# Kernel tuning notes

Measured on AMD Instinct MI355X. Metric: run time of the kernel, lower is better.

The kernel has to match this reference:

```python
import jax, jax.numpy as jnp
import numpy as np

B, S, D, H, DK, DV = 4, 2048, 512, 8, 64, 64


def setup_inputs() -> dict:
    key0 = jax.random.key(0)
    ks = jax.random.split(key0, 11)
    w = 0.02
    return {
        "query": jax.random.normal(ks[0], (B, S, D), dtype=jnp.float32),
        "key": jax.random.normal(ks[1], (B, S, D), dtype=jnp.float32),
        "value": jax.random.normal(ks[2], (B, S, D), dtype=jnp.float32),
        "Wq": jax.random.normal(ks[3], (D, DK), dtype=jnp.float32) * w,
        "bq": jnp.zeros((DK,), dtype=jnp.float32),
        "Wk": jax.random.normal(ks[4], (D, DK), dtype=jnp.float32) * w,
        "bk": jnp.zeros((DK,), dtype=jnp.float32),
        "Wv": jax.random.normal(ks[5], (D, DV), dtype=jnp.float32) * w,
        "bv": jnp.zeros((DV,), dtype=jnp.float32),
        "Wo": jax.random.normal(ks[6], (H * DV, D), dtype=jnp.float32) * w,
        "bo": jnp.zeros((D,), dtype=jnp.float32),
    }


def reference(query, key, value, Wq, bq, Wk, bk, Wv, bv, Wo, bo):
    # NOTE: original module applies the SAME Dense layers to every head
    # (q_list = [self.query(query) for _ in range(heads)]), so all H heads
    # are mathematically identical -> compute one head and replicate.
    # NOTE: V is projected from `key`, not `value` (faithful to source bug).
    q = query @ Wq + bq          # [B, S, DK]
    k = key @ Wk + bk            # [B, S, DK]
    v = key @ Wv + bv            # [B, S, DV]
    scale = np.sqrt(DK).astype(np.float32)
    scores = jnp.einsum("bqd,bkd->bqk", q, k) / scale  # [B, S, S]
    # masked_mha=True and training=True -> causal mask, fill -1e19
    causal = jnp.triu(jnp.ones((S, S), dtype=scores.dtype), 1)
    scores = scores + causal * jnp.asarray(-1e19, scores.dtype)
    attn = jax.nn.softmax(scores, axis=-1)              # [B, S, S]
    o = jnp.einsum("bqk,bkv->bqv", attn, v)             # [B, S, DV]
    # concat of H identical heads along last axis == tile
    concat = jnp.tile(o, (1, 1, H))                     # [B, S, H*DV]
    return concat @ Wo + bo                             # [B, S, D]
```

## Files before the change

### kernel.cpp

```cpp
#include <hip/hip_runtime.h>
#include <hip/hip_bf16.h>


#define BB 4
#define SS 2048
#define BS (BB*SS)

typedef __bf16          v8bf __attribute__((ext_vector_type(8)));
typedef unsigned short  v8u  __attribute__((ext_vector_type(8)));
typedef float           v4f  __attribute__((ext_vector_type(4)));

__device__ inline unsigned short f2bf(float x) {
    unsigned int u = __float_as_uint(x);
    return (unsigned short)((u + 0x7FFF + ((u >> 16) & 1)) >> 16);
}
__device__ inline float bf2f(unsigned short h) {
    return __uint_as_float((unsigned int)h << 16);
}
union bfcast { v8u u; v8bf b; };

__global__ __launch_bounds__(512) void prep_kernel(
    const float* __restrict__ Wq, const float* __restrict__ bq,
    const float* __restrict__ Wk, const float* __restrict__ bk,
    const float* __restrict__ Wv, const float* __restrict__ bv,
    const float* __restrict__ Wo,
    unsigned short* __restrict__ Wt, float* __restrict__ bs,
    unsigned short* __restrict__ WoEt)
{
    const int t = threadIdx.x, y = blockIdx.y;
    const int idx = blockIdx.x * 512 + t;
    if (y < 3) {
        const float* W  = (y == 0) ? Wq : (y == 1) ? Wk : Wv;
        const float* bb = (y == 0) ? bq : (y == 1) ? bk : bv;
        const float s = (y == 0) ? (0.125f * 1.44269504088896340736f) : 1.0f;
        int c = idx & 63, k = idx >> 6;
        Wt[y * 32768 + c * 512 + k] = f2bf(W[k * 64 + c] * s);
        if (blockIdx.x == 0 && t < 64) bs[y * 64 + t] = bb[t] * s;
    } else {
        int d = idx & 511, k = idx >> 9;
        float sum = 0.f;
#pragma unroll
        for (int h = 0; h < 8; h++) sum += Wo[(size_t)(h * 64 + k) * 512 + d];
        WoEt[d * 64 + k] = f2bf(sum);
    }
}

__global__ __launch_bounds__(256) void proj_kernel(
    const float* __restrict__ query, const float* __restrict__ key,
    const unsigned short* __restrict__ Wt, const float* __restrict__ bs,
    unsigned short* __restrict__ Qp, unsigned short* __restrict__ Kp,
    unsigned short* __restrict__ Vt)
{
    const int t = threadIdx.x;
    const int gw = (blockIdx.x * 256 + t) >> 6;
    const int lane = t & 63, lq = lane & 15, quad = lane >> 4;
    const int src = gw >> 11;
    const int rr  = gw & 2047;
    const int rows = (rr >> 2) * 16;
    const int cb   = (rr & 3) * 16;
    const float* A = (src == 0) ? query : key;
    const unsigned short* W = Wt + src * 32768 + (cb + lq) * 512;
    const float bb = bs[src * 64 + cb + lq];
    v4f acc = {bb, bb, bb, bb};
    const float* arow = A + (size_t)(rows + lq) * 512;

#pragma unroll 4
    for (int k0 = 0; k0 < 512; k0 += 32) {
        float4 f0 = *(const float4*)(arow + k0 + quad * 8);
        float4 f1 = *(const float4*)(arow + k0 + quad * 8 + 4);
        bfcast a;
        a.u[0] = f2bf(f0.x); a.u[1] = f2bf(f0.y); a.u[2] = f2bf(f0.z); a.u[3] = f2bf(f0.w);
        a.u[4] = f2bf(f1.x); a.u[5] = f2bf(f1.y); a.u[6] = f2bf(f1.z); a.u[7] = f2bf(f1.w);
        v8bf b = *(const v8bf*)(W + k0 + quad * 8);
        acc = __builtin_amdgcn_mfma_f32_16x16x32_bf16(a.b, b, acc, 0, 0, 0);
    }

    if (src == 2) {
        ushort4 o4;
        o4.x = f2bf(acc[0]); o4.y = f2bf(acc[1]); o4.z = f2bf(acc[2]); o4.w = f2bf(acc[3]);
        *(ushort4*)&Vt[(size_t)(cb + lq) * BS + rows + quad * 4] = o4;
    } else {
        unsigned short* Out = (src == 0) ? Qp : Kp;
#pragma unroll
        for (int r = 0; r < 4; r++)
            Out[(size_t)(rows + quad * 4 + r) * 64 + cb + lq] = f2bf(acc[r]);
    }
}

__global__ __launch_bounds__(256) void attn_kernel(
    const unsigned short* __restrict__ Qp,
    const unsigned short* __restrict__ Kp,
    const unsigned short* __restrict__ Vt,
    unsigned short* __restrict__ Opart,
    float* __restrict__ mpart, float* __restrict__ lpart,
    int nch)
{
    __shared__ unsigned short Ks[32][72];
    __shared__ unsigned short Vs[64][40];
    __shared__ unsigned short Ps[4][16][40];

    const int t    = threadIdx.x;
    const int lane = t & 63;
    const int w    = t >> 6;
    const int b    = blockIdx.x & 3;
    const int qt   = 31 - (blockIdx.x >> 2);
    const int c    = blockIdx.y;
    const int qbase = qt * 64;
    const int L    = qbase + 64;
    const int cs   = ((L + nch * 32 - 1) / (nch * 32)) * 32;
    const int klo  = c * cs;
    const int khi  = min(klo + cs, L);
    const size_t bbase = (size_t)b * SS;

    const int lq   = lane & 15;
    const int quad = lane >> 4;
    const int qrow_w = qbase + w * 16;
    const int wmax   = qrow_w + 15;

    const size_t qoff = (bbase + qrow_w + lq) * 64;
    v8bf qa0 = *(const v8bf*)(Qp + qoff + quad * 8);
    v8bf qa1 = *(const v8bf*)(Qp + qoff + 32 + quad * 8);

    v4f  o[4] = {};
    float mr[4], lr[4];
#pragma unroll
    for (int r = 0; r < 4; r++) { mr[r] = -1e30f; lr[r] = 0.f; }

    for (int kb = klo; kb < khi; kb += 32) {
        __syncthreads();
        {
            int ky = t >> 3, dd = (t & 7) * 8;
            *(v8bf*)&Ks[ky][dd] = *(const v8bf*)(Kp + (bbase + kb + ky) * 64 + dd);
            int vd = t >> 2, kk = (t & 3) * 8;
            *(v8bf*)&Vs[vd][kk] = *(const v8bf*)(Vt + (size_t)vd * BS + bbase + kb + kk);
        }
        __syncthreads();
        if (kb > wmax) continue;

        v4f s0 = {0.f, 0.f, 0.f, 0.f}, s1 = {0.f, 0.f, 0.f, 0.f};
        {
            v8bf k0a = *(const v8bf*)&Ks[lq][quad * 8];
            v8bf k0b = *(const v8bf*)&Ks[lq][32 + quad * 8];
            v8bf k1a = *(const v8bf*)&Ks[16 + lq][quad * 8];
            v8bf k1b = *(const v8bf*)&Ks[16 + lq][32 + quad * 8];
            s0 = __builtin_amdgcn_mfma_f32_16x16x32_bf16(qa0, k0a, s0, 0, 0, 0);
            s0 = __builtin_amdgcn_mfma_f32_16x16x32_bf16(qa1, k0b, s0, 0, 0, 0);
            s1 = __builtin_amdgcn_mfma_f32_16x16x32_bf16(qa0, k1a, s1, 0, 0, 0);
            s1 = __builtin_amdgcn_mfma_f32_16x16x32_bf16(qa1, k1b, s1, 0, 0, 0);
        }

        const int row0 = qrow_w + quad * 4;
        const int col0 = kb + lq;
        float sc[8];
#pragma unroll
        for (int r = 0; r < 4; r++) {
            sc[r]     = (col0      > row0 + r) ? -1e30f : s0[r];
            sc[4 + r] = (col0 + 16 > row0 + r) ? -1e30f : s1[r];
        }
        float mt[4];
#pragma unroll
        for (int r = 0; r < 4; r++) mt[r] = fmaxf(sc[r], sc[4 + r]);
#pragma unroll
        for (int off = 1; off <= 8; off <<= 1)
#pragma unroll
            for (int r = 0; r < 4; r++) mt[r] = fmaxf(mt[r], __shfl_xor(mt[r], off));

        float al[4], pn[8], ls[4];
#pragma unroll
        for (int r = 0; r < 4; r++) {
            float mn = fmaxf(mr[r], mt[r]);
            al[r] = exp2f(mr[r] - mn);
            mr[r] = mn;
            pn[r]     = exp2f(sc[r]     - mn);
            pn[4 + r] = exp2f(sc[4 + r] - mn);
            ls[r] = pn[r] + pn[4 + r];
        }
#pragma unroll
        for (int off = 1; off <= 8; off <<= 1)
#pragma unroll
            for (int r = 0; r < 4; r++) ls[r] += __shfl_xor(ls[r], off);
#pragma unroll
        for (int r = 0; r < 4; r++) lr[r] = lr[r] * al[r] + ls[r];

#pragma unroll
        for (int r = 0; r < 4; r++) {
            Ps[w][quad * 4 + r][lq]      = f2bf(pn[r]);
            Ps[w][quad * 4 + r][16 + lq] = f2bf(pn[4 + r]);
        }
        v8bf pa = *(const v8bf*)&Ps[w][lq][quad * 8];

#pragma unroll
        for (int vt = 0; vt < 4; vt++) {
            v8bf vb = *(const v8bf*)&Vs[vt * 16 + lq][quad * 8];
#pragma unroll
            for (int r = 0; r < 4; r++) o[vt][r] *= al[r];
            o[vt] = __builtin_amdgcn_mfma_f32_16x16x32_bf16(pa, vb, o[vt], 0, 0, 0);
        }
    }

#pragma unroll
    for (int vt = 0; vt < 4; vt++)
#pragma unroll
        for (int r = 0; r < 4; r++) {
            int qrow = qrow_w + quad * 4 + r;
            Opart[((size_t)c * BS + bbase + qrow) * 64 + vt * 16 + lq] = f2bf(o[vt][r]);
        }
    if (lq < 4) {
        int qrow = qrow_w + quad * 4 + lq;
        float mv = (lq == 0) ? mr[0] : (lq == 1) ? mr[1] : (lq == 2) ? mr[2] : mr[3];
        float lv = (lq == 0) ? lr[0] : (lq == 1) ? lr[1] : (lq == 2) ? lr[2] : lr[3];
        mpart[(size_t)c * BS + bbase + qrow] = mv;
        lpart[(size_t)c * BS + bbase + qrow] = lv;
    }
}

__global__ __launch_bounds__(256) void merge_kernel(
    const unsigned short* __restrict__ Opart, const float* __restrict__ mpart,
    const float* __restrict__ lpart, unsigned short* __restrict__ Om, int nch)
{
    const int idx = blockIdx.x * 256 + threadIdx.x;
    const int row = idx >> 3, dd = (idx & 7) * 8;
    float mm = -1e30f;
    for (int c = 0; c < nch; c++) mm = fmaxf(mm, mpart[(size_t)c * BS + row]);
    float den = 0.f;
    for (int c = 0; c < nch; c++)
        den += exp2f(mpart[(size_t)c * BS + row] - mm) * lpart[(size_t)c * BS + row];
    const float inv = 1.f / den;
    float acc[8] = {};
    for (int c = 0; c < nch; c++) {
        float s = exp2f(mpart[(size_t)c * BS + row] - mm) * inv;
        v8u o = *(const v8u*)&Opart[((size_t)c * BS + row) * 64 + dd];
#pragma unroll
        for (int j = 0; j < 8; j++) acc[j] += s * bf2f(o[j]);
    }
    v8u ou;
#pragma unroll
    for (int j = 0; j < 8; j++) ou[j] = f2bf(acc[j]);
    *(v8u*)&Om[(size_t)row * 64 + dd] = ou;
}

__global__ __launch_bounds__(256) void outgemm_kernel(
    const unsigned short* __restrict__ Om, const unsigned short* __restrict__ WoEt,
    const float* __restrict__ bo, float* __restrict__ out)
{
    const int t = threadIdx.x;
    const int gw = (blockIdx.x * 256 + t) >> 6;
    const int lane = t & 63, lq = lane & 15, quad = lane >> 4;
    const int rows = (gw >> 5) * 16;
    const int cb   = (gw & 31) * 16;

    v8bf a0 = *(const v8bf*)(Om + (size_t)(rows + lq) * 64 + quad * 8);
    v8bf a1 = *(const v8bf*)(Om + (size_t)(rows + lq) * 64 + 32 + quad * 8);
    v8bf b0 = *(const v8bf*)(WoEt + (size_t)(cb + lq) * 64 + quad * 8);
    v8bf b1 = *(const v8bf*)(WoEt + (size_t)(cb + lq) * 64 + 32 + quad * 8);
    const float bb = bo[cb + lq];
    v4f acc = {bb, bb, bb, bb};
    acc = __builtin_amdgcn_mfma_f32_16x16x32_bf16(a0, b0, acc, 0, 0, 0);
    acc = __builtin_amdgcn_mfma_f32_16x16x32_bf16(a1, b1, acc, 0, 0, 0);
#pragma unroll
    for (int r = 0; r < 4; r++)
        out[(size_t)(rows + quad * 4 + r) * 512 + cb + lq] = acc[r];
}

extern "C" void kernel_launch(void* const* d_in, const int* in_sizes, int n_in,
                              void* d_out, int out_size, void* d_ws, size_t ws_size,
                              hipStream_t stream) {
    const float* query = (const float*)d_in[0];
    const float* key   = (const float*)d_in[1];
    const float* Wq = (const float*)d_in[3];
    const float* bq = (const float*)d_in[4];
    const float* Wk = (const float*)d_in[5];
    const float* bk = (const float*)d_in[6];
    const float* Wv = (const float*)d_in[7];
    const float* bv = (const float*)d_in[8];
    const float* Wo = (const float*)d_in[9];
    const float* bo = (const float*)d_in[10];
    float* out = (float*)d_out;

    const int nch = (ws_size >= (size_t)13 * 1024 * 1024) ? 8 : 4;

    char* p = (char*)d_ws;
    unsigned short* Qp    = (unsigned short*)p; p += (size_t)BS * 64 * 2;
    unsigned short* Kp    = (unsigned short*)p; p += (size_t)BS * 64 * 2;
    unsigned short* Vtg   = (unsigned short*)p; p += (size_t)BS * 64 * 2;
    unsigned short* Opart = (unsigned short*)p; p += (size_t)nch * BS * 64 * 2;
    float* mpart = (float*)p; p += (size_t)nch * BS * 4;
    float* lpart = (float*)p; p += (size_t)nch * BS * 4;
    unsigned short* WoEt = (unsigned short*)p; p += (size_t)64 * 512 * 2;
    unsigned short* Wt   = (unsigned short*)p; p += (size_t)3 * 64 * 512 * 2;
    float* bs            = (float*)p;           p += (size_t)3 * 64 * 4;
    unsigned short* Om = Qp;

    prep_kernel<<<dim3(64, 4), 512, 0, stream>>>(Wq, bq, Wk, bk, Wv, bv, Wo, Wt, bs, WoEt);
    proj_kernel<<<1536, 256, 0, stream>>>(query, key, Wt, bs, Qp, Kp, Vtg);
    attn_kernel<<<dim3(128, nch), 256, 0, stream>>>(Qp, Kp, Vtg, Opart, mpart, lpart, nch);
    merge_kernel<<<256, 256, 0, stream>>>(Opart, mpart, lpart, Om, nch);
    outgemm_kernel<<<4096, 256, 0, stream>>>(Om, WoEt, bo, out);
}
```

Measured before the change: 182.1 us.

## Fuse K/V projections, widen attention key tile, merge combine with output GEMM

The projection kernel now computes K and V from the same key rows in one wave, so each key row is loaded and converted to bf16 once instead of twice. The attention kernel processes 64-key tiles instead of 32, which halves the number of barrier-synchronised tile iterations at the cost of larger shared buffers. The split-K merge and the output GEMM are fused into one kernel, which drops a launch and the intermediate Om round trip through global memory. Hand-rolled bf16 rounding is replaced by native __bf16 conversions.

```diff
diff --git a/kernel.cpp b/kernel.cpp
--- a/kernel.cpp
+++ b/kernel.cpp
@@ -6,26 +6,24 @@
 #define SS 2048
 #define BS (BB*SS)
 
-typedef __bf16          v8bf __attribute__((ext_vector_type(8)));
-typedef unsigned short  v8u  __attribute__((ext_vector_type(8)));
-typedef float           v4f  __attribute__((ext_vector_type(4)));
-
-__device__ inline unsigned short f2bf(float x) {
-    unsigned int u = __float_as_uint(x);
-    return (unsigned short)((u + 0x7FFF + ((u >> 16) & 1)) >> 16);
-}
-__device__ inline float bf2f(unsigned short h) {
-    return __uint_as_float((unsigned int)h << 16);
-}
-union bfcast { v8u u; v8bf b; };
+typedef __bf16 v8bf __attribute__((ext_vector_type(8)));
+typedef __bf16 v4bf __attribute__((ext_vector_type(4)));
+typedef float  v4f  __attribute__((ext_vector_type(4)));
+
+__device__ inline v8bf cvt8(float4 f0, float4 f1) {
+    v8bf r;
+    r[0] = (__bf16)f0.x; r[1] = (__bf16)f0.y; r[2] = (__bf16)f0.z; r[3] = (__bf16)f0.w;
+    r[4] = (__bf16)f1.x; r[5] = (__bf16)f1.y; r[6] = (__bf16)f1.z; r[7] = (__bf16)f1.w;
+    return r;
+}
 
 __global__ __launch_bounds__(512) void prep_kernel(
     const float* __restrict__ Wq, const float* __restrict__ bq,
     const float* __restrict__ Wk, const float* __restrict__ bk,
     const float* __restrict__ Wv, const float* __restrict__ bv,
     const float* __restrict__ Wo,
-    unsigned short* __restrict__ Wt, float* __restrict__ bs,
-    unsigned short* __restrict__ WoEt)
+    __bf16* __restrict__ Wt, float* __restrict__ bs,
+    __bf16* __restrict__ WoEt)
 {
     const int t = threadIdx.x, y = blockIdx.y;
     const int idx = blockIdx.x * 512 + t;
@@ -34,70 +32,81 @@
         const float* bb = (y == 0) ? bq : (y == 1) ? bk : bv;
         const float s = (y == 0) ? (0.125f * 1.44269504088896340736f) : 1.0f;
         int c = idx & 63, k = idx >> 6;
-        Wt[y * 32768 + c * 512 + k] = f2bf(W[k * 64 + c] * s);
+        Wt[y * 32768 + c * 512 + k] = (__bf16)(W[k * 64 + c] * s);
         if (blockIdx.x == 0 && t < 64) bs[y * 64 + t] = bb[t] * s;
     } else {
         int d = idx & 511, k = idx >> 9;
         float sum = 0.f;
 #pragma unroll
         for (int h = 0; h < 8; h++) sum += Wo[(size_t)(h * 64 + k) * 512 + d];
-        WoEt[d * 64 + k] = f2bf(sum);
+        WoEt[d * 64 + k] = (__bf16)sum;
     }
 }
 
 __global__ __launch_bounds__(256) void proj_kernel(
     const float* __restrict__ query, const float* __restrict__ key,
-    const unsigned short* __restrict__ Wt, const float* __restrict__ bs,
-    unsigned short* __restrict__ Qp, unsigned short* __restrict__ Kp,
-    unsigned short* __restrict__ Vt)
+    const __bf16* __restrict__ Wt, const float* __restrict__ bs,
+    __bf16* __restrict__ Qp, __bf16* __restrict__ Kp, __bf16* __restrict__ Vt)
 {
     const int t = threadIdx.x;
     const int gw = (blockIdx.x * 256 + t) >> 6;
     const int lane = t & 63, lq = lane & 15, quad = lane >> 4;
-    const int src = gw >> 11;
+    const int kind = gw >> 11;
     const int rr  = gw & 2047;
     const int rows = (rr >> 2) * 16;
     const int cb   = (rr & 3) * 16;
-    const float* A = (src == 0) ? query : key;
-    const unsigned short* W = Wt + src * 32768 + (cb + lq) * 512;
-    const float bb = bs[src * 64 + cb + lq];
-    v4f acc = {bb, bb, bb, bb};
-    const float* arow = A + (size_t)(rows + lq) * 512;
-
+    const float* arow = ((kind == 0) ? query : key) + (size_t)(rows + lq) * 512;
+
+    if (kind == 0) {
+        const __bf16* W = Wt + (cb + lq) * 512;
+        const float bb = bs[cb + lq];
+        v4f acc = {bb, bb, bb, bb};
 #pragma unroll 4
-    for (int k0 = 0; k0 < 512; k0 += 32) {
-        float4 f0 = *(const float4*)(arow + k0 + quad * 8);
-        float4 f1 = *(const float4*)(arow + k0 + quad * 8 + 4);
-        bfcast a;
-        a.u[0] = f2bf(f0.x); a.u[1] = f2bf(f0.y); a.u[2] = f2bf(f0.z); a.u[3] = f2bf(f0.w);
-        a.u[4] = f2bf(f1.x); a.u[5] = f2bf(f1.y); a.u[6] = f2bf(f1.z); a.u[7] = f2bf(f1.w);
-        v8bf b = *(const v8bf*)(W + k0 + quad * 8);
-        acc = __builtin_amdgcn_mfma_f32_16x16x32_bf16(a.b, b, acc, 0, 0, 0);
-    }
-
-    if (src == 2) {
-        ushort4 o4;
-        o4.x = f2bf(acc[0]); o4.y = f2bf(acc[1]); o4.z = f2bf(acc[2]); o4.w = f2bf(acc[3]);
-        *(ushort4*)&Vt[(size_t)(cb + lq) * BS + rows + quad * 4] = o4;
+        for (int k0 = 0; k0 < 512; k0 += 32) {
+            float4 f0 = *(const float4*)(arow + k0 + quad * 8);
+            float4 f1 = *(const float4*)(arow + k0 + quad * 8 + 4);
+            v8bf a = cvt8(f0, f1);
+            v8bf b = *(const v8bf*)(W + k0 + quad * 8);
+            acc = __builtin_amdgcn_mfma_f32_16x16x32_bf16(a, b, acc, 0, 0, 0);
+        }
+#pragma unroll
+        for (int r = 0; r < 4; r++)
+            Qp[(size_t)(rows + quad * 4 + r) * 64 + cb + lq] = (__bf16)acc[r];
     } else {
-        unsigned short* Out = (src == 0) ? Qp : Kp;
+        const __bf16* Wk_ = Wt + 32768  + (cb + lq) * 512;
+        const __bf16* Wv_ = Wt + 65536  + (cb + lq) * 512;
+        const float bk_ = bs[64 + cb + lq], bv_ = bs[128 + cb + lq];
+        v4f ak = {bk_, bk_, bk_, bk_}, av = {bv_, bv_, bv_, bv_};
+#pragma unroll 4
+        for (int k0 = 0; k0 < 512; k0 += 32) {
+            float4 f0 = *(const float4*)(arow + k0 + quad * 8);
+            float4 f1 = *(const float4*)(arow + k0 + quad * 8 + 4);
+            v8bf a  = cvt8(f0, f1);
+            v8bf b0 = *(const v8bf*)(Wk_ + k0 + quad * 8);
+            v8bf b1 = *(const v8bf*)(Wv_ + k0 + quad * 8);
+            ak = __builtin_amdgcn_mfma_f32_16x16x32_bf16(a, b0, ak, 0, 0, 0);
+            av = __builtin_amdgcn_mfma_f32_16x16x32_bf16(a, b1, av, 0, 0, 0);
+        }
 #pragma unroll
         for (int r = 0; r < 4; r++)
-            Out[(size_t)(rows + quad * 4 + r) * 64 + cb + lq] = f2bf(acc[r]);
+            Kp[(size_t)(rows + quad * 4 + r) * 64 + cb + lq] = (__bf16)ak[r];
+        v4bf o4; o4[0] = (__bf16)av[0]; o4[1] = (__bf16)av[1];
+        o4[2] = (__bf16)av[2]; o4[3] = (__bf16)av[3];
+        *(v4bf*)&Vt[(size_t)(cb + lq) * BS + rows + quad * 4] = o4;
     }
 }
 
 __global__ __launch_bounds__(256) void attn_kernel(
-    const unsigned short* __restrict__ Qp,
-    const unsigned short* __restrict__ Kp,
-    const unsigned short* __restrict__ Vt,
-    unsigned short* __restrict__ Opart,
+    const __bf16* __restrict__ Qp,
+    const __bf16* __restrict__ Kp,
+    const __bf16* __restrict__ Vt,
+    __bf16* __restrict__ Opart,
     float* __restrict__ mpart, float* __restrict__ lpart,
     int nch)
 {
-    __shared__ unsigned short Ks[32][72];
-    __shared__ unsigned short Vs[64][40];
-    __shared__ unsigned short Ps[4][16][40];
+    __shared__ __bf16 Ks[64][72];
+    __shared__ __bf16 Vs[64][72];
+    __shared__ __bf16 Ps[4][16][72];
 
     const int t    = threadIdx.x;
     const int lane = t & 63;
@@ -107,7 +116,7 @@
     const int c    = blockIdx.y;
     const int qbase = qt * 64;
     const int L    = qbase + 64;
-    const int cs   = ((L + nch * 32 - 1) / (nch * 32)) * 32;
+    const int cs   = ((L + nch * 64 - 1) / (nch * 64)) * 64;
     const int klo  = c * cs;
     const int khi  = min(klo + cs, L);
     const size_t bbase = (size_t)b * SS;
@@ -126,54 +135,56 @@
 #pragma unroll
     for (int r = 0; r < 4; r++) { mr[r] = -1e30f; lr[r] = 0.f; }
 
-    for (int kb = klo; kb < khi; kb += 32) {
+    for (int kb = klo; kb < khi; kb += 64) {
         __syncthreads();
-        {
-            int ky = t >> 3, dd = (t & 7) * 8;
+#pragma unroll
+        for (int i = 0; i < 2; i++) {
+            int idx = t + i * 256;
+            int ky = idx >> 3, dd = (idx & 7) * 8;
             *(v8bf*)&Ks[ky][dd] = *(const v8bf*)(Kp + (bbase + kb + ky) * 64 + dd);
-            int vd = t >> 2, kk = (t & 3) * 8;
-            *(v8bf*)&Vs[vd][kk] = *(const v8bf*)(Vt + (size_t)vd * BS + bbase + kb + kk);
+            *(v8bf*)&Vs[ky][dd] = *(const v8bf*)(Vt + (size_t)ky * BS + bbase + kb + dd);
         }
         __syncthreads();
         if (kb > wmax) continue;
 
-        v4f s0 = {0.f, 0.f, 0.f, 0.f}, s1 = {0.f, 0.f, 0.f, 0.f};
-        {
-            v8bf k0a = *(const v8bf*)&Ks[lq][quad * 8];
-            v8bf k0b = *(const v8bf*)&Ks[lq][32 + quad * 8];
-            v8bf k1a = *(const v8bf*)&Ks[16 + lq][quad * 8];
-            v8bf k1b = *(const v8bf*)&Ks[16 + lq][32 + quad * 8];
-            s0 = __builtin_amdgcn_mfma_f32_16x16x32_bf16(qa0, k0a, s0, 0, 0, 0);
-            s0 = __builtin_amdgcn_mfma_f32_16x16x32_bf16(qa1, k0b, s0, 0, 0, 0);
-            s1 = __builtin_amdgcn_mfma_f32_16x16x32_bf16(qa0, k1a, s1, 0, 0, 0);
-            s1 = __builtin_amdgcn_mfma_f32_16x16x32_bf16(qa1, k1b, s1, 0, 0, 0);
+        v4f s[4];
+#pragma unroll
+        for (int n = 0; n < 4; n++) {
+            v8bf ka = *(const v8bf*)&Ks[n * 16 + lq][quad * 8];
+            v8bf kb2 = *(const v8bf*)&Ks[n * 16 + lq][32 + quad * 8];
+            v4f z = {0.f, 0.f, 0.f, 0.f};
+            z = __builtin_amdgcn_mfma_f32_16x16x32_bf16(qa0, ka, z, 0, 0, 0);
+            s[n] = __builtin_amdgcn_mfma_f32_16x16x32_bf16(qa1, kb2, z, 0, 0, 0);
         }
 
         const int row0 = qrow_w + quad * 4;
         const int col0 = kb + lq;
-        float sc[8];
-#pragma unroll
-        for (int r = 0; r < 4; r++) {
-            sc[r]     = (col0      > row0 + r) ? -1e30f : s0[r];
-            sc[4 + r] = (col0 + 16 > row0 + r) ? -1e30f : s1[r];
-        }
+        float sc[4][4];
+#pragma unroll
+        for (int n = 0; n < 4; n++)
+#pragma unroll
+            for (int r = 0; r < 4; r++)
+                sc[n][r] = (col0 + n * 16 > row0 + r) ? -1e30f : s[n][r];
+
         float mt[4];
 #pragma unroll
-        for (int r = 0; r < 4; r++) mt[r] = fmaxf(sc[r], sc[4 + r]);
+        for (int r = 0; r < 4; r++)
+            mt[r] = fmaxf(fmaxf(sc[0][r], sc[1][r]), fmaxf(sc[2][r], sc[3][r]));
 #pragma unroll
         for (int off = 1; off <= 8; off <<= 1)
 #pragma unroll
             for (int r = 0; r < 4; r++) mt[r] = fmaxf(mt[r], __shfl_xor(mt[r], off));
 
-        float al[4], pn[8], ls[4];
+        float al[4], pn[4][4], ls[4];
 #pragma unroll
         for (int r = 0; r < 4; r++) {
             float mn = fmaxf(mr[r], mt[r]);
             al[r] = exp2f(mr[r] - mn);
             mr[r] = mn;
-            pn[r]     = exp2f(sc[r]     - mn);
-            pn[4 + r] = exp2f(sc[4 + r] - mn);
-            ls[r] = pn[r] + pn[4 + r];
+            float t0 = 0.f;
+#pragma unroll
+            for (int n = 0; n < 4; n++) { pn[n][r] = exp2f(sc[n][r] - mn); t0 += pn[n][r]; }
+            ls[r] = t0;
         }
 #pragma unroll
         for (int off = 1; off <= 8; off <<= 1)
@@ -183,18 +194,21 @@
         for (int r = 0; r < 4; r++) lr[r] = lr[r] * al[r] + ls[r];
 
 #pragma unroll
-        for (int r = 0; r < 4; r++) {
-            Ps[w][quad * 4 + r][lq]      = f2bf(pn[r]);
-            Ps[w][quad * 4 + r][16 + lq] = f2bf(pn[4 + r]);
-        }
-        v8bf pa = *(const v8bf*)&Ps[w][lq][quad * 8];
+        for (int n = 0; n < 4; n++)
+#pragma unroll
+            for (int r = 0; r < 4; r++)
+                Ps[w][quad * 4 + r][n * 16 + lq] = (__bf16)pn[n][r];
+        v8bf pa0 = *(const v8bf*)&Ps[w][lq][quad * 8];
+        v8bf pa1 = *(const v8bf*)&Ps[w][lq][32 + quad * 8];
 
 #pragma unroll
         for (int vt = 0; vt < 4; vt++) {
-            v8bf vb = *(const v8bf*)&Vs[vt * 16 + lq][quad * 8];
+            v8bf vb0 = *(const v8bf*)&Vs[vt * 16 + lq][quad * 8];
+            v8bf vb1 = *(const v8bf*)&Vs[vt * 16 + lq][32 + quad * 8];
 #pragma unroll
             for (int r = 0; r < 4; r++) o[vt][r] *= al[r];
-            o[vt] = __builtin_amdgcn_mfma_f32_16x16x32_bf16(pa, vb, o[vt], 0, 0, 0);
+            o[vt] = __builtin_amdgcn_mfma_f32_16x16x32_bf16(pa0, vb0, o[vt], 0, 0, 0);
+            o[vt] = __builtin_amdgcn_mfma_f32_16x16x32_bf16(pa1, vb1, o[vt], 0, 0, 0);
         }
     }
 
@@ -203,7 +217,7 @@
 #pragma unroll
         for (int r = 0; r < 4; r++) {
             int qrow = qrow_w + quad * 4 + r;
-            Opart[((size_t)c * BS + bbase + qrow) * 64 + vt * 16 + lq] = f2bf(o[vt][r]);
+            Opart[((size_t)c * BS + bbase + qrow) * 64 + vt * 16 + lq] = (__bf16)o[vt][r];
         }
     if (lq < 4) {
         int qrow = qrow_w + quad * 4 + lq;
@@ -214,52 +228,59 @@
     }
 }
 
-__global__ __launch_bounds__(256) void merge_kernel(
-    const unsigned short* __restrict__ Opart, const float* __restrict__ mpart,
-    const float* __restrict__ lpart, unsigned short* __restrict__ Om, int nch)
+__global__ __launch_bounds__(256) void outmerge_kernel(
+    const __bf16* __restrict__ Opart, const float* __restrict__ mpart,
+    const float* __restrict__ lpart, const __bf16* __restrict__ WoEt,
+    const float* __restrict__ bo, float* __restrict__ out, int nch)
 {
-    const int idx = blockIdx.x * 256 + threadIdx.x;
-    const int row = idx >> 3, dd = (idx & 7) * 8;
-    float mm = -1e30f;
-    for (int c = 0; c < nch; c++) mm = fmaxf(mm, mpart[(size_t)c * BS + row]);
-    float den = 0.f;
-    for (int c = 0; c < nch; c++)
-        den += exp2f(mpart[(size_t)c * BS + row] - mm) * lpart[(size_t)c * BS + row];
-    const float inv = 1.f / den;
-    float acc[8] = {};
-    for (int c = 0; c < nch; c++) {
-        float s = exp2f(mpart[(size_t)c * BS + row] - mm) * inv;
-        v8u o = *(const v8u*)&Opart[((size_t)c * BS + row) * 64 + dd];
-#pragma unroll
-        for (int j = 0; j < 8; j++) acc[j] += s * bf2f(o[j]);
-    }
-    v8u ou;
-#pragma unroll
-    for (int j = 0; j < 8; j++) ou[j] = f2bf(acc[j]);
-    *(v8u*)&Om[(size_t)row * 64 + dd] = ou;
-}
-
-__global__ __launch_bounds__(256) void outgemm_kernel(
-    const unsigned short* __restrict__ Om, const unsigned short* __restrict__ WoEt,
-    const float* __restrict__ bo, float* __restrict__ out)
-{
+    __shared__ __bf16 Os[16][72];
+    __shared__ float wgt[8][16];
     const int t = threadIdx.x;
-    const int gw = (blockIdx.x * 256 + t) >> 6;
+    const int rows0 = blockIdx.x * 16;
+
+    if (t < 16) {
+        int row = rows0 + t;
+        float mm = -1e30f;
+        for (int c = 0; c < nch; c++) mm = fmaxf(mm, mpart[(size_t)c * BS + row]);
+        float den = 0.f;
+        for (int c = 0; c < nch; c++)
+            den += exp2f(mpart[(size_t)c * BS + row] - mm) * lpart[(size_t)c * BS + row];
+        float invd = 1.f / den;
+        for (int c = 0; c < nch; c++)
+            wgt[c][t] = exp2f(mpart[(size_t)c * BS + row] - mm) * invd;
+    }
+    __syncthreads();
+    {
+        int row = t >> 4, d0 = (t & 15) * 4;
+        float a0 = 0.f, a1 = 0.f, a2 = 0.f, a3 = 0.f;
+        for (int c = 0; c < nch; c++) {
+            float s = wgt[c][row];
+            v4bf v = *(const v4bf*)&Opart[((size_t)c * BS + rows0 + row) * 64 + d0];
+            a0 += s * (float)v[0]; a1 += s * (float)v[1];
+            a2 += s * (float)v[2]; a3 += s * (float)v[3];
+        }
+        Os[row][d0] = (__bf16)a0; Os[row][d0 + 1] = (__bf16)a1;
+        Os[row][d0 + 2] = (__bf16)a2; Os[row][d0 + 3] = (__bf16)a3;
+    }
+    __syncthreads();
+
     const int lane = t & 63, lq = lane & 15, quad = lane >> 4;
-    const int rows = (gw >> 5) * 16;
-    const int cb   = (gw & 31) * 16;
-
-    v8bf a0 = *(const v8bf*)(Om + (size_t)(rows + lq) * 64 + quad * 8);
-    v8bf a1 = *(const v8bf*)(Om + (size_t)(rows + lq) * 64 + 32 + quad * 8);
-    v8bf b0 = *(const v8bf*)(WoEt + (size_t)(cb + lq) * 64 + quad * 8);
-    v8bf b1 = *(const v8bf*)(WoEt + (size_t)(cb + lq) * 64 + 32 + quad * 8);
-    const float bb = bo[cb + lq];
-    v4f acc = {bb, bb, bb, bb};
-    acc = __builtin_amdgcn_mfma_f32_16x16x32_bf16(a0, b0, acc, 0, 0, 0);
-    acc = __builtin_amdgcn_mfma_f32_16x16x32_bf16(a1, b1, acc, 0, 0, 0);
-#pragma unroll
-    for (int r = 0; r < 4; r++)
-        out[(size_t)(rows + quad * 4 + r) * 512 + cb + lq] = acc[r];
+    const int w = t >> 6;
+    v8bf a0 = *(const v8bf*)&Os[lq][quad * 8];
+    v8bf a1 = *(const v8bf*)&Os[lq][32 + quad * 8];
+#pragma unroll
+    for (int i = 0; i < 8; i++) {
+        const int cb = (w * 8 + i) * 16;
+        v8bf b0 = *(const v8bf*)(WoEt + (size_t)(cb + lq) * 64 + quad * 8);
+        v8bf b1 = *(const v8bf*)(WoEt + (size_t)(cb + lq) * 64 + 32 + quad * 8);
+        const float bb = bo[cb + lq];
+        v4f acc = {bb, bb, bb, bb};
+        acc = __builtin_amdgcn_mfma_f32_16x16x32_bf16(a0, b0, acc, 0, 0, 0);
+        acc = __builtin_amdgcn_mfma_f32_16x16x32_bf16(a1, b1, acc, 0, 0, 0);
+#pragma unroll
+        for (int r = 0; r < 4; r++)
+            out[(size_t)(rows0 + quad * 4 + r) * 512 + cb + lq] = acc[r];
+    }
 }
 
 extern "C" void kernel_launch(void* const* d_in, const int* in_sizes, int n_in,
@@ -280,20 +301,18 @@
     const int nch = (ws_size >= (size_t)13 * 1024 * 1024) ? 8 : 4;
 
     char* p = (char*)d_ws;
-    unsigned short* Qp    = (unsigned short*)p; p += (size_t)BS * 64 * 2;
-    unsigned short* Kp    = (unsigned short*)p; p += (size_t)BS * 64 * 2;
-    unsigned short* Vtg   = (unsigned short*)p; p += (size_t)BS * 64 * 2;
-    unsigned short* Opart = (unsigned short*)p; p += (size_t)nch * BS * 64 * 2;
+    __bf16* Qp    = (__bf16*)p; p += (size_t)BS * 64 * 2;
+    __bf16* Kp    = (__bf16*)p; p += (size_t)BS * 64 * 2;
+    __bf16* Vtg   = (__bf16*)p; p += (size_t)BS * 64 * 2;
+    __bf16* Opart = (__bf16*)p; p += (size_t)nch * BS * 64 * 2;
     float* mpart = (float*)p; p += (size_t)nch * BS * 4;
     float* lpart = (float*)p; p += (size_t)nch * BS * 4;
-    unsigned short* WoEt = (unsigned short*)p; p += (size_t)64 * 512 * 2;
-    unsigned short* Wt   = (unsigned short*)p; p += (size_t)3 * 64 * 512 * 2;
-    float* bs            = (float*)p;           p += (size_t)3 * 64 * 4;
-    unsigned short* Om = Qp;
+    __bf16* WoEt = (__bf16*)p; p += (size_t)64 * 512 * 2;
+    __bf16* Wt   = (__bf16*)p; p += (size_t)3 * 64 * 512 * 2;
+    float* bs    = (float*)p;  p += (size_t)3 * 64 * 4;
 
     prep_kernel<<<dim3(64, 4), 512, 0, stream>>>(Wq, bq, Wk, bk, Wv, bv, Wo, Wt, bs, WoEt);
-    proj_kernel<<<1536, 256, 0, stream>>>(query, key, Wt, bs, Qp, Kp, Vtg);
+    proj_kernel<<<1024, 256, 0, stream>>>(query, key, Wt, bs, Qp, Kp, Vtg);
     attn_kernel<<<dim3(128, nch), 256, 0, stream>>>(Qp, Kp, Vtg, Opart, mpart, lpart, nch);
-    merge_kernel<<<256, 256, 0, stream>>>(Opart, mpart, lpart, Om, nch);
-    outgemm_kernel<<<4096, 256, 0, stream>>>(Om, WoEt, bo, out);
-}
+    outmerge_kernel<<<512, 256, 0, stream>>>(Opart, mpart, lpart, WoEt, bo, out, nch);
+}
```

After: 156.8 us. 1.16x faster.
